# Optimization experiments

Measured on AMD Instinct MI355X. Metric: run time of the kernel, lower is better.

The kernel has to match this reference:

```python
import jax, jax.numpy as jnp
import numpy as np

B, T, C = 8, 1024, 512
H = 8
E = C // 2  # split_idx == per-head dim e


def setup_inputs() -> dict:
    key = jax.random.key(0)
    ks = jax.random.split(key, 6)
    s = 0.02
    return {
        "x": jax.random.normal(ks[0], (B, T, C), dtype=jnp.float32),
        "Wq": jax.random.normal(ks[1], (E * H, E), dtype=jnp.float32) * s,
        "Wk": jax.random.normal(ks[2], (E * H, E), dtype=jnp.float32) * s,
        "Wv": jax.random.normal(ks[3], (E * H, E), dtype=jnp.float32) * s,
        "Wu": jax.random.normal(ks[4], (C - E, E * H), dtype=jnp.float32) * s,
        "bu": jnp.zeros((C - E,), dtype=jnp.float32),
    }


def reference(x, Wq, Wk, Wv, Wu, bu):
    # coupling split: x1 drives attention, x2 gets additive update
    x1 = x[..., :E]           # [B,T,E]
    x2 = x[..., E:]           # [B,T,C-E]
    scale = E ** (-0.25)
    # torch Linear: y = x W^T ; output viewed as (heads, e) -> heads-major rows
    q = jnp.einsum('bti,oi->bto', x1, Wq).reshape(B, T, H, E) * scale
    k = jnp.einsum('bti,oi->bto', x1, Wk).reshape(B, T, H, E) * scale
    v = jnp.einsum('bti,oi->bto', x1, Wv).reshape(B, T, H, E)
    # attention scores [B,H,T,T]
    dot = jnp.einsum('bthe,bshe->bhts', q, k)
    attn = jax.nn.softmax(dot, axis=-1)
    out = jnp.einsum('bhts,bshe->bthe', attn, v).reshape(B, T, H * E)
    unified = jnp.einsum('bto,co->btc', out, Wu) + bu  # [B,T,C-E]
    return jnp.concatenate([x1, x2 + unified], axis=-1)
```

## Files before the change

### kernel.cpp

```cpp
#include <hip/hip_runtime.h>
#include <hip/hip_bf16.h>

#define BB 8
#define TT 1024
#define CC 512
#define HH 8
#define EE 256
#define MM (BB*TT)
#define HE (HH*EE)

using short8 = __attribute__((ext_vector_type(8))) short;
using f32x16 = __attribute__((ext_vector_type(16))) float;
using uint2v = __attribute__((ext_vector_type(2))) unsigned int;

__device__ __forceinline__ unsigned short f2bf(float f) {
  union { float f; unsigned int i; } v; v.f = f;
  unsigned int r = v.i + 0x7FFFu + ((v.i >> 16) & 1u);
  return (unsigned short)(r >> 16);
}
__device__ __forceinline__ unsigned int pk_bf16(float lo, float hi) {
  unsigned int r;
  asm("v_cvt_pk_bf16_f32 %0, %1, %2" : "=v"(r) : "v"(lo), "v"(hi));
  return r;
}
__device__ __forceinline__ void gll16(const void* g, void* l) {
  __builtin_amdgcn_global_load_lds(
      (const __attribute__((address_space(1))) unsigned int*)g,
      (__attribute__((address_space(3))) unsigned int*)l, 16, 0, 0);
}

__global__ __launch_bounds__(256) void prep_kernel(const float* __restrict__ x,
                                                   const float* __restrict__ Wq,
                                                   const float* __restrict__ Wk,
                                                   const float* __restrict__ Wv,
                                                   unsigned short* __restrict__ xb,
                                                   unsigned short* __restrict__ wf,
                                                   float* __restrict__ out) {
  int t = blockIdx.x * 256 + threadIdx.x;
  if (t < 262144) {
    int m = t >> 5;
    int c8 = (t & 31) * 8;
    float4 a = *reinterpret_cast<const float4*>(&x[(size_t)m * CC + c8]);
    float4 b = *reinterpret_cast<const float4*>(&x[(size_t)m * CC + c8 + 4]);
    union { unsigned int u[4]; short8 v; } o;
    o.u[0] = pk_bf16(a.x, a.y); o.u[1] = pk_bf16(a.z, a.w);
    o.u[2] = pk_bf16(b.x, b.y); o.u[3] = pk_bf16(b.z, b.w);
    *reinterpret_cast<short8*>(&xb[(size_t)m * 256 + c8]) = o.v;
    *reinterpret_cast<float4*>(&out[(size_t)m * CC + c8]) = a;
    *reinterpret_cast<float4*>(&out[(size_t)m * CC + c8 + 4]) = b;
  } else {
    int t2 = t - 262144;
    int lane = t2 & 63;
    int rest = t2 >> 6;
    int ks = rest & 15;
    int ng = (rest >> 4) & 63;
    int w = rest >> 10;
    const float* Wp = (w == 0) ? Wq : (w == 1) ? Wk : Wv;
    const float scl = (w == 0) ? 0.25f * 1.44269504089f : (w == 1) ? 0.25f : 1.0f;
    int n = ng * 32 + (lane & 31);
    int e0 = ks * 16 + (lane >> 5) * 8;
    float4 a = *reinterpret_cast<const float4*>(&Wp[(size_t)n * EE + e0]);
    float4 b = *reinterpret_cast<const float4*>(&Wp[(size_t)n * EE + e0 + 4]);
    union { unsigned int u[4]; short8 v; } o;
    o.u[0] = pk_bf16(a.x * scl, a.y * scl); o.u[1] = pk_bf16(a.z * scl, a.w * scl);
    o.u[2] = pk_bf16(b.x * scl, b.y * scl); o.u[3] = pk_bf16(b.z * scl, b.w * scl);
    *reinterpret_cast<short8*>(&wf[(size_t)t2 * 8]) = o.v;
  }
}

__global__ __launch_bounds__(256) void qkv_static_kernel(const unsigned short* __restrict__ xb,
                                                         const unsigned short* __restrict__ wf,
                                                         unsigned short* __restrict__ outq,
                                                         unsigned short* __restrict__ outk,
                                                         unsigned short* __restrict__ outvt) {
  __shared__ unsigned short Ab[64 * 256];

  const int tid = threadIdx.x;
  const int lane = tid & 63;
  const int wid = tid >> 6;
  const int wc = wid;
  const int lo = lane & 31, hi = lane >> 5;

  int bid = blockIdx.x;
  int r = bid >> 3;
  int mt = (bid & 7) * 16 + (r & 15);
  int nt = r >> 4;
  const int m0 = mt * 64;
  const int n0 = nt * 128;

  {
    const int a_sub = lane >> 5;
    const int a_g = lane & 31;
#pragma unroll
    for (int i = 0; i < 8; ++i) {
      int row = 16 * wid + 2 * i + a_sub;
      int gs = a_g ^ (row & 7);
      gll16(xb + (size_t)(m0 + row) * 256 + gs * 8, Ab + (16 * wid + 2 * i) * 256);
    }
  }
  asm volatile("s_waitcnt vmcnt(0)" ::: "memory");
  __builtin_amdgcn_s_barrier();

  f32x16 acc[3][2];
#pragma unroll
  for (int w = 0; w < 3; ++w)
#pragma unroll
    for (int mi = 0; mi < 2; ++mi)
#pragma unroll
      for (int q = 0; q < 16; ++q) acc[w][mi][q] = 0.f;

  const int ng = nt * 4 + wc;
  const short8* wfp = reinterpret_cast<const short8*>(wf);
  const int sxor = lo & 7;

#pragma unroll
  for (int ks = 0; ks < 16; ++ks) {
    short8 bf[3];
#pragma unroll
    for (int w = 0; w < 3; ++w)
      bf[w] = wfp[(size_t)((w * 64 + ng) * 16 + ks) * 64 + lane];
    short8 af[2];
#pragma unroll
    for (int mi = 0; mi < 2; ++mi) {
      int row = 32 * mi + lo;
      int slot = (ks * 2 + hi) ^ sxor;
      af[mi] = *reinterpret_cast<const short8*>(&Ab[row * 256 + slot * 8]);
    }
#pragma unroll
    for (int w = 0; w < 3; ++w)
#pragma unroll
      for (int mi = 0; mi < 2; ++mi)
        acc[w][mi] = __builtin_amdgcn_mfma_f32_32x32x16_bf16(af[mi], bf[w], acc[w][mi], 0, 0, 0);
  }

  unsigned short* Tq = Ab;
  const int erow_r = tid >> 4;
  const int en8 = (tid & 15) * 8;
#pragma unroll
  for (int w = 0; w < 2; ++w) {
    unsigned short* op = (w == 0) ? outq : outk;
    __syncthreads();
#pragma unroll
    for (int mi = 0; mi < 2; ++mi)
#pragma unroll
      for (int q = 0; q < 16; ++q) {
        int rr = (q & 3) + 8 * (q >> 2) + 4 * hi;
        Tq[(32 * mi + rr) * 140 + 32 * wc + lo] = f2bf(acc[w][mi][q]);
      }
    __syncthreads();
#pragma unroll
    for (int p = 0; p < 4; ++p) {
      int row = p * 16 + erow_r;
      *reinterpret_cast<short8*>(&op[(size_t)(m0 + row) * HE + n0 + en8]) =
          *reinterpret_cast<const short8*>(&Tq[row * 140 + en8]);
    }
  }

  unsigned short* Tr = Ab;
  __syncthreads();
#pragma unroll
  for (int mi = 0; mi < 2; ++mi)
#pragma unroll
    for (int q = 0; q < 16; ++q) {
      int rr = (q & 3) + 8 * (q >> 2) + 4 * hi;
      Tr[(32 * wc + lo) * 72 + 32 * mi + rr] = f2bf(acc[2][mi][q]);
    }
  __syncthreads();
  {
    const int b = m0 >> 10;
    const int t0m = m0 & 1023;
#pragma unroll
    for (int p = 0; p < 4; ++p) {
      int nr = p * 32 + (tid >> 3);
      int chunk = tid & 7;
      int n = n0 + nr;
      size_t drow = ((size_t)b * 8 + (n >> 8)) * 256 + (n & 255);
      *reinterpret_cast<short8*>(&outvt[drow * TT + t0m + chunk * 8]) =
          *reinterpret_cast<const short8*>(&Tr[nr * 72 + chunk * 8]);
    }
  }
}

#define SBLK 32
__global__ __launch_bounds__(256, 2) void attn_kernel(const unsigned short* __restrict__ qg,
                                                      const unsigned short* __restrict__ kg,
                                                      const unsigned short* __restrict__ vtg,
                                                      unsigned short* __restrict__ og) {
  __shared__ char smem[66048];
  unsigned short* Kbuf = (unsigned short*)smem;
  unsigned short* Vbuf = (unsigned short*)(smem + 32768);
  float* lpart = (float*)(smem + 65536);

  const int tid = threadIdx.x;
  const int lane = tid & 63;
  const int wid = tid >> 6;
  const int lo = lane & 31, hi = lane >> 5;

  int logical = (blockIdx.x & 7) * 64 + (blockIdx.x >> 3);
  const int bh = logical >> 3;
  const int t0 = (logical & 7) * 128;
  const int b = bh >> 3, h = bh & 7;
  const size_t qkbase = (size_t)b * TT * HE + (size_t)h * EE;
  const size_t vtbase = (size_t)bh * EE * TT;
  const unsigned short* kg_base = kg + qkbase;
  const unsigned short* vt_base = vtg + vtbase;

  short8 qf[16];
  {
    const unsigned short* qrow = qg + qkbase + (size_t)(t0 + 32 * wid + lo) * HE + hi * 8;
#pragma unroll
    for (int ks = 0; ks < 16; ++ks)
      qf[ks] = *reinterpret_cast<const short8*>(qrow + ks * 16);
  }

  f32x16 Oacc[8];
#pragma unroll
  for (int et = 0; et < 8; ++et)
#pragma unroll
    for (int q = 0; q < 16; ++q) Oacc[et][q] = 0.f;
  float lacc = 0.f;

  const int k_sub = lane >> 5;
  const int k_g   = lane & 31;
  const int v_er  = lane >> 2;
  const int v_g   = lane & 3;
  const int v_gs  = v_g ^ ((lane >> 3) & 3);

#define STAGE_TILE(TIDX, BUF)                                                        \
  {                                                                                  \
    const unsigned short* kt = kg_base + (size_t)(TIDX) * SBLK * HE;                 \
    const unsigned short* vt = vt_base + (size_t)(TIDX) * SBLK;                      \
    unsigned short* Kb = Kbuf + (BUF) * (SBLK * 256);                                \
    unsigned short* Vb = Vbuf + (BUF) * (256 * SBLK);                                \
    _Pragma("unroll")                                                                \
    for (int i = 0; i < 4; ++i) {                                                    \
      int row = 8 * wid + 2 * i + k_sub;                                             \
      int gs = k_g ^ (row & 7);                                                      \
      gll16(kt + (size_t)row * HE + gs * 8, Kb + (8 * wid + 2 * i) * 256);           \
    }                                                                                \
    _Pragma("unroll")                                                                \
    for (int i = 0; i < 4; ++i) {                                                    \
      int row = 64 * wid + 16 * i + v_er;                                            \
      gll16(vt + (size_t)row * TT + v_gs * 8, Vb + (64 * wid + 16 * i) * SBLK);      \
    }                                                                                \
  }

  STAGE_TILE(0, 0)
  asm volatile("s_waitcnt vmcnt(0)" ::: "memory");
  __builtin_amdgcn_s_barrier();
  __builtin_amdgcn_sched_barrier(0);

  for (int t = 0; t < 32; ++t) {
    const int cur = t & 1;
    if (t + 1 < 32) STAGE_TILE(t + 1, cur ^ 1)

    const unsigned short* Kb = Kbuf + cur * (SBLK * 256);
    const unsigned short* Vb = Vbuf + cur * (256 * SBLK);

    f32x16 sacc;
#pragma unroll
    for (int q = 0; q < 16; ++q) sacc[q] = 0.f;
    const int sxor = lo & 7;
#pragma unroll
    for (int ks = 0; ks < 16; ++ks) {
      int slot = (ks * 2 + hi) ^ sxor;
      short8 kf = *reinterpret_cast<const short8*>(&Kb[lo * 256 + slot * 8]);
      sacc = __builtin_amdgcn_mfma_f32_32x32x16_bf16(kf, qf[ks], sacc, 0, 0, 0);
    }

    short8 pa[2];
#pragma unroll
    for (int ksl = 0; ksl < 2; ++ksl) {
      float p0 = __builtin_amdgcn_exp2f(sacc[8 * ksl + 0]);
      float p1 = __builtin_amdgcn_exp2f(sacc[8 * ksl + 1]);
      float p2 = __builtin_amdgcn_exp2f(sacc[8 * ksl + 2]);
      float p3 = __builtin_amdgcn_exp2f(sacc[8 * ksl + 3]);
      float p4 = __builtin_amdgcn_exp2f(sacc[8 * ksl + 4]);
      float p5 = __builtin_amdgcn_exp2f(sacc[8 * ksl + 5]);
      float p6 = __builtin_amdgcn_exp2f(sacc[8 * ksl + 6]);
      float p7 = __builtin_amdgcn_exp2f(sacc[8 * ksl + 7]);
      lacc += ((p0 + p1) + (p2 + p3)) + ((p4 + p5) + (p6 + p7));
      unsigned int a1 = pk_bf16(p0, p1), a2 = pk_bf16(p2, p3);
      unsigned int b1 = pk_bf16(p4, p5), b2 = pk_bf16(p6, p7);
      uint2v r1 = __builtin_amdgcn_permlane32_swap(a1, b1, false, false);
      uint2v r2 = __builtin_amdgcn_permlane32_swap(a2, b2, false, false);
      union { unsigned int u[4]; short8 v; } uu;
      uu.u[0] = r1[0]; uu.u[1] = r2[0]; uu.u[2] = r1[1]; uu.u[3] = r2[1];
      pa[ksl] = uu.v;
    }

    const int vxor = (lo >> 1) & 3;
#pragma unroll
    for (int et = 0; et < 8; ++et) {
      const int erow = et * 32 + lo;
#pragma unroll
      for (int ksl = 0; ksl < 2; ++ksl) {
        int slot = (2 * ksl + hi) ^ vxor;
        short8 vf = *reinterpret_cast<const short8*>(&Vb[erow * SBLK + slot * 8]);
        Oacc[et] = __builtin_amdgcn_mfma_f32_32x32x16_bf16(pa[ksl], vf, Oacc[et], 0, 0, 0);
      }
    }

    asm volatile("s_waitcnt vmcnt(0)" ::: "memory");
    __builtin_amdgcn_s_barrier();
    __builtin_amdgcn_sched_barrier(0);
  }

  lacc += __shfl_xor(lacc, 32);
  if (hi == 0) lpart[wid * 32 + lo] = lacc;
  __syncthreads();
#pragma unroll
  for (int q = 0; q < 16; ++q) {
    int rr = (q & 3) + 8 * (q >> 2) + 4 * hi;
    float inv = 1.0f / lpart[wid * 32 + rr];
    int tq = t0 + 32 * wid + rr;
#pragma unroll
    for (int et = 0; et < 8; ++et)
      og[qkbase + (size_t)tq * HE + et * 32 + lo] = f2bf(Oacc[et][q] * inv);
  }
#undef STAGE_TILE
}

#define PSTR 72
__global__ __launch_bounds__(256) void proj_mfma_kernel(const unsigned short* __restrict__ ao,
                                                        const float* __restrict__ Wu,
                                                        const float* __restrict__ bu,
                                                        const float* __restrict__ x,
                                                        float* __restrict__ out) {
  __shared__ unsigned short As[64 * PSTR];
  __shared__ unsigned short Bs[64 * PSTR];
  const int tid = threadIdx.x;
  const int lane = tid & 63;
  const int wid = tid >> 6;
  const int wr = wid >> 1, wc = wid & 1;
  const int lo = lane & 31, hi = lane >> 5;

  int bid = blockIdx.x;
  int r = bid >> 3;
  int mt = (bid & 7) * 16 + (r & 15);
  int nt = r >> 4;
  const int m0 = mt * 64;
  const int n0 = nt * 64;

  const int arow = tid >> 2;
  const int ag0 = (tid & 3) * 2;
  const int brow = tid >> 2;
  const int bg0 = (tid & 3) * 4;

  short8 raA[2];
  float4 raB[4];
  f32x16 acc;
#pragma unroll
  for (int q = 0; q < 16; ++q) acc[q] = 0.f;

#pragma unroll
  for (int j = 0; j < 2; ++j)
    raA[j] = *reinterpret_cast<const short8*>(&ao[(size_t)(m0 + arow) * HE + (ag0 + j) * 8]);
#pragma unroll
  for (int g = 0; g < 4; ++g)
    raB[g] = *reinterpret_cast<const float4*>(&Wu[(size_t)(n0 + brow) * HE + (bg0 + g) * 4]);

  for (int t = 0; t < 32; ++t) {
#pragma unroll
    for (int j = 0; j < 2; ++j)
      *reinterpret_cast<short8*>(&As[arow * PSTR + (ag0 + j) * 8]) = raA[j];
    {
      union { unsigned int u[4]; short8 v; } w0, w1;
      w0.u[0] = pk_bf16(raB[0].x, raB[0].y); w0.u[1] = pk_bf16(raB[0].z, raB[0].w);
      w0.u[2] = pk_bf16(raB[1].x, raB[1].y); w0.u[3] = pk_bf16(raB[1].z, raB[1].w);
      w1.u[0] = pk_bf16(raB[2].x, raB[2].y); w1.u[1] = pk_bf16(raB[2].z, raB[2].w);
      w1.u[2] = pk_bf16(raB[3].x, raB[3].y); w1.u[3] = pk_bf16(raB[3].z, raB[3].w);
      *reinterpret_cast<short8*>(&Bs[brow * PSTR + ag0 * 8]) = w0.v;
      *reinterpret_cast<short8*>(&Bs[brow * PSTR + (ag0 + 1) * 8]) = w1.v;
    }
    asm volatile("s_waitcnt lgkmcnt(0)" ::: "memory");
    __builtin_amdgcn_s_barrier();
    __builtin_amdgcn_sched_barrier(0);

    if (t + 1 < 32) {
      int k0 = (t + 1) * 64;
#pragma unroll
      for (int j = 0; j < 2; ++j)
        raA[j] = *reinterpret_cast<const short8*>(&ao[(size_t)(m0 + arow) * HE + k0 + (ag0 + j) * 8]);
#pragma unroll
      for (int g = 0; g < 4; ++g)
        raB[g] = *reinterpret_cast<const float4*>(&Wu[(size_t)(n0 + brow) * HE + k0 + (bg0 + g) * 4]);
    }

    __builtin_amdgcn_s_setprio(1);
#pragma unroll
    for (int ks = 0; ks < 4; ++ks) {
      short8 af = *reinterpret_cast<const short8*>(&As[(32 * wr + lo) * PSTR + ks * 16 + hi * 8]);
      short8 bf = *reinterpret_cast<const short8*>(&Bs[(32 * wc + lo) * PSTR + ks * 16 + hi * 8]);
      acc = __builtin_amdgcn_mfma_f32_32x32x16_bf16(af, bf, acc, 0, 0, 0);
    }
    __builtin_amdgcn_s_setprio(0);
    __builtin_amdgcn_s_barrier();
    __builtin_amdgcn_sched_barrier(0);
  }

  {
    int n = n0 + 32 * wc + lo;
    float bias = bu[n];
#pragma unroll
    for (int q = 0; q < 16; ++q) {
      int rr = (q & 3) + 8 * (q >> 2) + 4 * hi;
      int m = m0 + 32 * wr + rr;
      float o = acc[q] + x[(size_t)m * CC + EE + n] + bias;
      out[(size_t)m * CC + EE + n] = o;
    }
  }
}

extern "C" void kernel_launch(void* const* d_in, const int* in_sizes, int n_in,
                              void* d_out, int out_size, void* d_ws, size_t ws_size,
                              hipStream_t stream) {
  const float* x  = (const float*)d_in[0];
  const float* Wq = (const float*)d_in[1];
  const float* Wk = (const float*)d_in[2];
  const float* Wv = (const float*)d_in[3];
  const float* Wu = (const float*)d_in[4];
  const float* bu = (const float*)d_in[5];
  float* out = (float*)d_out;

  unsigned short* q  = (unsigned short*)d_ws;
  unsigned short* k  = q + (size_t)MM * HE;
  unsigned short* vt = k + (size_t)MM * HE;
  unsigned short* ao = vt + (size_t)MM * HE;
  unsigned short* xb = ao;
  unsigned short* wfb = xb + (size_t)MM * EE;

  prep_kernel<<<dim3(1792), dim3(256), 0, stream>>>(x, Wq, Wk, Wv, xb, wfb, out);

  qkv_static_kernel<<<dim3(2048), dim3(256), 0, stream>>>(xb, wfb, q, k, vt);

  attn_kernel<<<dim3(512), dim3(256), 0, stream>>>(q, k, vt, ao);

  proj_mfma_kernel<<<dim3(512), dim3(256), 0, stream>>>(ao, Wu, bu, x, out);
}
```

Measured before the change: 155.1 us.

## Store K and V in MFMA fragment order so attention loads contiguous tiles

The QKV kernel now writes K and V directly in the per-lane MFMA operand layout, tiled per 32-key block. The attention kernel can then stage each tile with fully contiguous 16-byte global-to-LDS loads and read fragments at lane*8 offsets without XOR swizzles. This cuts address arithmetic and makes global reads fully coalesced in the attention loop. In exchange the QKV epilogue does more scattered-address stores, and unswizzled LDS reads could hit bank conflicts.

```diff
diff --git a/kernel.cpp b/kernel.cpp
--- a/kernel.cpp
+++ b/kernel.cpp
@@ -28,6 +28,7 @@
       (const __attribute__((address_space(1))) unsigned int*)g,
       (__attribute__((address_space(3))) unsigned int*)l, 16, 0, 0);
 }
+
 
 __global__ __launch_bounds__(256) void prep_kernel(const float* __restrict__ x,
                                                    const float* __restrict__ Wq,
@@ -71,8 +72,8 @@
 __global__ __launch_bounds__(256) void qkv_static_kernel(const unsigned short* __restrict__ xb,
                                                          const unsigned short* __restrict__ wf,
                                                          unsigned short* __restrict__ outq,
-                                                         unsigned short* __restrict__ outk,
-                                                         unsigned short* __restrict__ outvt) {
+                                                         unsigned short* __restrict__ kfrag,
+                                                         unsigned short* __restrict__ vfrag) {
   __shared__ unsigned short Ab[64 * 256];
 
   const int tid = threadIdx.x;
@@ -133,58 +134,84 @@
         acc[w][mi] = __builtin_amdgcn_mfma_f32_32x32x16_bf16(af[mi], bf[w], acc[w][mi], 0, 0, 0);
   }
 
+  const int bh = (m0 >> 10) * 8 + (n0 >> 8);
+  const int stile0 = (m0 & 1023) >> 5;
+
   unsigned short* Tq = Ab;
-  const int erow_r = tid >> 4;
-  const int en8 = (tid & 15) * 8;
-#pragma unroll
-  for (int w = 0; w < 2; ++w) {
-    unsigned short* op = (w == 0) ? outq : outk;
+  {
     __syncthreads();
 #pragma unroll
     for (int mi = 0; mi < 2; ++mi)
 #pragma unroll
       for (int q = 0; q < 16; ++q) {
         int rr = (q & 3) + 8 * (q >> 2) + 4 * hi;
-        Tq[(32 * mi + rr) * 140 + 32 * wc + lo] = f2bf(acc[w][mi][q]);
+        Tq[(32 * mi + rr) * 140 + 32 * wc + lo] = f2bf(acc[0][mi][q]);
       }
     __syncthreads();
+    const int erow_r = tid >> 4;
+    const int en8 = (tid & 15) * 8;
 #pragma unroll
     for (int p = 0; p < 4; ++p) {
       int row = p * 16 + erow_r;
-      *reinterpret_cast<short8*>(&op[(size_t)(m0 + row) * HE + n0 + en8]) =
+      *reinterpret_cast<short8*>(&outq[(size_t)(m0 + row) * HE + n0 + en8]) =
           *reinterpret_cast<const short8*>(&Tq[row * 140 + en8]);
     }
   }
 
+  {
+    __syncthreads();
+#pragma unroll
+    for (int mi = 0; mi < 2; ++mi)
+#pragma unroll
+      for (int q = 0; q < 16; ++q) {
+        int rr = (q & 3) + 8 * (q >> 2) + 4 * hi;
+        Tq[(32 * mi + rr) * 140 + 32 * wc + lo] = f2bf(acc[1][mi][q]);
+      }
+    __syncthreads();
+#pragma unroll
+    for (int j = 0; j < 4; ++j) {
+      int slot = j * 256 + tid;
+      int l64 = slot & 63, lo64 = l64 & 31, hi64 = l64 >> 5;
+      int rest = slot >> 6;
+      int ksl_ = rest & 7, stl = rest >> 3;
+      short8 vv = *reinterpret_cast<const short8*>(
+          &Tq[(stl * 32 + lo64) * 140 + ksl_ * 16 + hi64 * 8]);
+      int ks_g = ((n0 & 255) >> 4) + ksl_;
+      size_t dst = (((size_t)(bh * 32 + stile0 + stl) * 16 + ks_g) * 64 + l64) * 8;
+      *reinterpret_cast<short8*>(&kfrag[dst]) = vv;
+    }
+  }
+
   unsigned short* Tr = Ab;
-  __syncthreads();
-#pragma unroll
-  for (int mi = 0; mi < 2; ++mi)
-#pragma unroll
-    for (int q = 0; q < 16; ++q) {
-      int rr = (q & 3) + 8 * (q >> 2) + 4 * hi;
-      Tr[(32 * wc + lo) * 72 + 32 * mi + rr] = f2bf(acc[2][mi][q]);
-    }
-  __syncthreads();
-  {
-    const int b = m0 >> 10;
-    const int t0m = m0 & 1023;
-#pragma unroll
-    for (int p = 0; p < 4; ++p) {
-      int nr = p * 32 + (tid >> 3);
-      int chunk = tid & 7;
-      int n = n0 + nr;
-      size_t drow = ((size_t)b * 8 + (n >> 8)) * 256 + (n & 255);
-      *reinterpret_cast<short8*>(&outvt[drow * TT + t0m + chunk * 8]) =
-          *reinterpret_cast<const short8*>(&Tr[nr * 72 + chunk * 8]);
-    }
-  }
-}
-
-#define SBLK 32
+  {
+    __syncthreads();
+#pragma unroll
+    for (int mi = 0; mi < 2; ++mi)
+#pragma unroll
+      for (int q = 0; q < 16; ++q) {
+        int rr = (q & 3) + 8 * (q >> 2) + 4 * hi;
+        Tr[(32 * wc + lo) * 72 + 32 * mi + rr] = f2bf(acc[2][mi][q]);
+      }
+    __syncthreads();
+#pragma unroll
+    for (int j = 0; j < 4; ++j) {
+      int slot = j * 256 + tid;
+      int l64 = slot & 63, lo64 = l64 & 31, hi64 = l64 >> 5;
+      int rest = slot >> 6;
+      int et_l = rest & 3, ksl = (rest >> 2) & 1, stl = rest >> 3;
+      short8 vv = *reinterpret_cast<const short8*>(
+          &Tr[(et_l * 32 + lo64) * 72 + stl * 32 + ksl * 16 + hi64 * 8]);
+      int et_g = ((n0 & 255) >> 5) + et_l;
+      size_t dst = ((((size_t)(bh * 32 + stile0 + stl) * 8 + et_g) * 2 + ksl) * 64 + l64) * 8;
+      *reinterpret_cast<short8*>(&vfrag[dst]) = vv;
+    }
+  }
+}
+
+#define TILE_EL 8192
 __global__ __launch_bounds__(256, 2) void attn_kernel(const unsigned short* __restrict__ qg,
-                                                      const unsigned short* __restrict__ kg,
-                                                      const unsigned short* __restrict__ vtg,
+                                                      const unsigned short* __restrict__ kfrag,
+                                                      const unsigned short* __restrict__ vfrag,
                                                       unsigned short* __restrict__ og) {
   __shared__ char smem[66048];
   unsigned short* Kbuf = (unsigned short*)smem;
@@ -195,15 +222,15 @@
   const int lane = tid & 63;
   const int wid = tid >> 6;
   const int lo = lane & 31, hi = lane >> 5;
+  const int l8 = lane * 8;
 
   int logical = (blockIdx.x & 7) * 64 + (blockIdx.x >> 3);
   const int bh = logical >> 3;
   const int t0 = (logical & 7) * 128;
   const int b = bh >> 3, h = bh & 7;
   const size_t qkbase = (size_t)b * TT * HE + (size_t)h * EE;
-  const size_t vtbase = (size_t)bh * EE * TT;
-  const unsigned short* kg_base = kg + qkbase;
-  const unsigned short* vt_base = vtg + vtbase;
+  const unsigned short* kf_base = kfrag + (size_t)bh * 32 * TILE_EL;
+  const unsigned short* vf_base = vfrag + (size_t)bh * 32 * TILE_EL;
 
   short8 qf[16];
   {
@@ -220,28 +247,17 @@
     for (int q = 0; q < 16; ++q) Oacc[et][q] = 0.f;
   float lacc = 0.f;
 
-  const int k_sub = lane >> 5;
-  const int k_g   = lane & 31;
-  const int v_er  = lane >> 2;
-  const int v_g   = lane & 3;
-  const int v_gs  = v_g ^ ((lane >> 3) & 3);
-
 #define STAGE_TILE(TIDX, BUF)                                                        \
   {                                                                                  \
-    const unsigned short* kt = kg_base + (size_t)(TIDX) * SBLK * HE;                 \
-    const unsigned short* vt = vt_base + (size_t)(TIDX) * SBLK;                      \
-    unsigned short* Kb = Kbuf + (BUF) * (SBLK * 256);                                \
-    unsigned short* Vb = Vbuf + (BUF) * (256 * SBLK);                                \
+    const unsigned short* kt = kf_base + (size_t)(TIDX) * TILE_EL;                   \
+    const unsigned short* vt = vf_base + (size_t)(TIDX) * TILE_EL;                   \
+    unsigned short* Kb = Kbuf + (BUF) * TILE_EL;                                     \
+    unsigned short* Vb = Vbuf + (BUF) * TILE_EL;                                     \
     _Pragma("unroll")                                                                \
     for (int i = 0; i < 4; ++i) {                                                    \
-      int row = 8 * wid + 2 * i + k_sub;                                             \
-      int gs = k_g ^ (row & 7);                                                      \
-      gll16(kt + (size_t)row * HE + gs * 8, Kb + (8 * wid + 2 * i) * 256);           \
-    }                                                                                \
-    _Pragma("unroll")                                                                \
-    for (int i = 0; i < 4; ++i) {                                                    \
-      int row = 64 * wid + 16 * i + v_er;                                            \
-      gll16(vt + (size_t)row * TT + v_gs * 8, Vb + (64 * wid + 16 * i) * SBLK);      \
+      int c = 4 * wid + i;                                                           \
+      gll16(kt + c * 512 + l8, Kb + c * 512);                                        \
+      gll16(vt + c * 512 + l8, Vb + c * 512);                                        \
     }                                                                                \
   }
 
@@ -254,17 +270,15 @@
     const int cur = t & 1;
     if (t + 1 < 32) STAGE_TILE(t + 1, cur ^ 1)
 
-    const unsigned short* Kb = Kbuf + cur * (SBLK * 256);
-    const unsigned short* Vb = Vbuf + cur * (256 * SBLK);
+    const unsigned short* Kb = Kbuf + cur * TILE_EL;
+    const unsigned short* Vb = Vbuf + cur * TILE_EL;
 
     f32x16 sacc;
 #pragma unroll
     for (int q = 0; q < 16; ++q) sacc[q] = 0.f;
-    const int sxor = lo & 7;
 #pragma unroll
     for (int ks = 0; ks < 16; ++ks) {
-      int slot = (ks * 2 + hi) ^ sxor;
-      short8 kf = *reinterpret_cast<const short8*>(&Kb[lo * 256 + slot * 8]);
+      short8 kf = *reinterpret_cast<const short8*>(&Kb[ks * 512 + l8]);
       sacc = __builtin_amdgcn_mfma_f32_32x32x16_bf16(kf, qf[ks], sacc, 0, 0, 0);
     }
 
@@ -289,14 +303,11 @@
       pa[ksl] = uu.v;
     }
 
-    const int vxor = (lo >> 1) & 3;
 #pragma unroll
     for (int et = 0; et < 8; ++et) {
-      const int erow = et * 32 + lo;
 #pragma unroll
       for (int ksl = 0; ksl < 2; ++ksl) {
-        int slot = (2 * ksl + hi) ^ vxor;
-        short8 vf = *reinterpret_cast<const short8*>(&Vb[erow * SBLK + slot * 8]);
+        short8 vf = *reinterpret_cast<const short8*>(&Vb[(et * 2 + ksl) * 512 + l8]);
         Oacc[et] = __builtin_amdgcn_mfma_f32_32x32x16_bf16(pa[ksl], vf, Oacc[et], 0, 0, 0);
       }
     }
@@ -423,18 +434,18 @@
   const float* bu = (const float*)d_in[5];
   float* out = (float*)d_out;
 
-  unsigned short* q  = (unsigned short*)d_ws;
-  unsigned short* k  = q + (size_t)MM * HE;
-  unsigned short* vt = k + (size_t)MM * HE;
-  unsigned short* ao = vt + (size_t)MM * HE;
-  unsigned short* xb = ao;
-  unsigned short* wfb = xb + (size_t)MM * EE;
+  unsigned short* q     = (unsigned short*)d_ws;
+  unsigned short* kfrag = q + (size_t)MM * HE;
+  unsigned short* vfrag = kfrag + (size_t)MM * HE;
+  unsigned short* ao    = vfrag + (size_t)MM * HE;
+  unsigned short* xb    = ao;
+  unsigned short* wfb   = xb + (size_t)MM * EE;
 
   prep_kernel<<<dim3(1792), dim3(256), 0, stream>>>(x, Wq, Wk, Wv, xb, wfb, out);
 
-  qkv_static_kernel<<<dim3(2048), dim3(256), 0, stream>>>(xb, wfb, q, k, vt);
-
-  attn_kernel<<<dim3(512), dim3(256), 0, stream>>>(q, k, vt, ao);
+  qkv_static_kernel<<<dim3(2048), dim3(256), 0, stream>>>(xb, wfb, q, kfrag, vfrag);
+
+  attn_kernel<<<dim3(512), dim3(256), 0, stream>>>(q, kfrag, vfrag, ao);
 
   proj_mfma_kernel<<<dim3(512), dim3(256), 0, stream>>>(ao, Wu, bu, x, out);
 }
```

New measurement: 141.6 us. 1.1x faster.
